# Optimization experiments

Measured on AMD Instinct MI355X. Metric: run time of the kernel, lower is better.

The kernel has to match this reference:

```python
import jax, jax.numpy as jnp
import numpy as np

N_HEAD = 16
T_THRESHOLD = 0.001


def setup_inputs() -> dict:
    key = jax.random.key(0)
    k_x, k_wa, k_ba, k_wp, k_bp = jax.random.split(key, 5)
    B, P, L, R = 8, 1024, 4, 256
    C = L * R  # n_embd = 1024
    s = 1.0 / np.sqrt(C)
    return {
        "x": jax.random.normal(k_x, (B, P, L, R), dtype=jnp.float32),
        "w_attn": jax.random.normal(k_wa, (C, 3 * C), dtype=jnp.float32) * s,
        "b_attn": jax.random.normal(k_ba, (3 * C,), dtype=jnp.float32) * 0.01,
        "w_proj": jax.random.normal(k_wp, (C, C), dtype=jnp.float32) * s,
        "b_proj": jax.random.normal(k_bp, (C,), dtype=jnp.float32) * 0.01,
    }


def reference(x, w_attn, b_attn, w_proj, b_proj):
    B, P, L, R = x.shape
    C = L * R
    H = N_HEAD
    hd = C // H
    xf = x.reshape(B, P, C)                      # (B, T, C)
    qkv = xf @ w_attn + b_attn                   # (B, T, 3C)
    q, k, v = jnp.split(qkv, 3, axis=-1)
    # (B, H, T, hd)
    q = q.reshape(B, P, H, hd).transpose(0, 2, 1, 3)
    k = k.reshape(B, P, H, hd).transpose(0, 2, 1, 3)
    v = v.reshape(B, P, H, hd).transpose(0, 2, 1, 3)
    att = jnp.einsum("bhqd,bhkd->bhqk", q, k) * (1.0 / np.sqrt(hd))
    att = jax.nn.softmax(att, axis=-1)
    att = jax.nn.relu(att - T_THRESHOLD)         # post-softmax thresholding
    y = jnp.einsum("bhqk,bhkd->bhqd", att, v)    # (B, H, T, hd)
    y = y.transpose(0, 2, 1, 3).reshape(B, P, C)
    y = y @ w_proj + b_proj
    return y.reshape(B, P, L, R)
```

## Files before the change

kernel.cpp:

```cpp
#include <hip/hip_runtime.h>


typedef _Float16 half8 __attribute__((ext_vector_type(8)));
typedef _Float16 half4_t __attribute__((ext_vector_type(4)));
typedef float floatx4 __attribute__((ext_vector_type(4)));

__device__ __forceinline__ void gl2lds16(const void* gsrc, void* lds) {
    __builtin_amdgcn_global_load_lds(
        (const __attribute__((address_space(1))) unsigned int*)gsrc,
        (__attribute__((address_space(3))) unsigned int*)lds,
        16, 0, 0);
}

__global__ __launch_bounds__(256) void conv_x(const float4* __restrict__ in,
                                              _Float16* __restrict__ out, int n4) {
    int idx = blockIdx.x * blockDim.x + threadIdx.x;
    int stride = gridDim.x * blockDim.x;
    for (int i = idx; i < n4; i += stride) {
        float4 v = in[i];
        half4_t h = { (_Float16)v.x, (_Float16)v.y, (_Float16)v.z, (_Float16)v.w };
        *(half4_t*)(out + (size_t)i * 4) = h;
    }
}

__global__ __launch_bounds__(256) void tconv2(const float* __restrict__ wa,
                                              _Float16* __restrict__ waT,
                                              const float* __restrict__ wp,
                                              _Float16* __restrict__ wpT) {
    __shared__ _Float16 t[64 * 65];
    int bx = blockIdx.x, by = blockIdx.y;
    const float* in = wa; _Float16* out = waT; int C = 3072;
    if (bx >= 48) { bx -= 48; in = wp; out = wpT; C = 1024; }
#pragma unroll
    for (int it = 0; it < 16; ++it) {
        int idx = it * 256 + threadIdx.x;
        int r = idx >> 6, c = idx & 63;
        t[c * 65 + r] = (_Float16)in[(size_t)(by * 64 + r) * C + bx * 64 + c];
    }
    __syncthreads();
#pragma unroll
    for (int it = 0; it < 16; ++it) {
        int idx = it * 256 + threadIdx.x;
        int rn = idx >> 6, ck = idx & 63;
        out[(size_t)(bx * 64 + rn) * 1024 + by * 64 + ck] = t[rn * 65 + ck];
    }
}

#define GBAR __builtin_amdgcn_s_barrier()
#define WLGKM do { asm volatile("s_waitcnt lgkmcnt(0)" ::: "memory"); } while (0)
#define WVM2  do { asm volatile("s_waitcnt vmcnt(2)"   ::: "memory"); } while (0)
#define WVM4  do { asm volatile("s_waitcnt vmcnt(4)"   ::: "memory"); } while (0)
#define WVM0  do { asm volatile("s_waitcnt vmcnt(0)"   ::: "memory"); } while (0)


#define WLDA(buf, rg)                                                                         \
    do {                                                                                      \
        _Pragma("unroll") for (int i = 0; i < 4; ++i) {                                       \
            int r_ = wm * 128 + ((rg) * 4 + i) * 16 + l15;                                    \
            _Pragma("unroll") for (int kk = 0; kk < 2; ++kk)                                  \
                a[i][kk] = *(const half8*)(sA + (buf) * 32768 + r_ * 128 +                    \
                                           ((((kk << 2) + quad) ^ (r_ & 7)) << 4));           \
        }                                                                                     \
    } while (0)

#define WLDB(buf, cg, bb)                                                                     \
    do {                                                                                      \
        _Pragma("unroll") for (int j = 0; j < 2; ++j) {                                       \
            int r_ = wn * 64 + ((cg) * 2 + j) * 16 + l15;                                     \
            _Pragma("unroll") for (int kk = 0; kk < 2; ++kk)                                  \
                bb[j][kk] = *(const half8*)(sB + (buf) * 32768 + r_ * 128 +                   \
                                            ((((kk << 2) + quad) ^ (r_ & 7)) << 4));          \
        }                                                                                     \
    } while (0)

#define WMMA(rg, cg, bb)                                                                      \
    do {                                                                                      \
        __builtin_amdgcn_s_setprio(1);                                                        \
        _Pragma("unroll") for (int kk = 0; kk < 2; ++kk)                                      \
            _Pragma("unroll") for (int i = 0; i < 4; ++i)                                     \
                _Pragma("unroll") for (int j = 0; j < 2; ++j)                                  \
                    acc[(rg) * 4 + i][(cg) * 2 + j] = __builtin_amdgcn_mfma_f32_16x16x32_f16( \
                        a[i][kk], bb[j][kk], acc[(rg) * 4 + i][(cg) * 2 + j], 0, 0, 0);       \
        __builtin_amdgcn_s_setprio(0);                                                        \
    } while (0)

__global__ __launch_bounds__(512, 2) void gemm_qkv(const _Float16* __restrict__ A,
                                                   const _Float16* __restrict__ BT,
                                                   const float* __restrict__ bias,
                                                   _Float16* __restrict__ qno,
                                                   _Float16* __restrict__ kPo,
                                                   _Float16* __restrict__ vPo) {
    __shared__ __attribute__((aligned(16))) char lds[131072];
    char* sA = lds;
    char* sB = lds + 65536;
    int tid = threadIdx.x;
    int W = tid >> 6, lane = tid & 63, quad = lane >> 4, l15 = lane & 15;
    int wm = W >> 2, wn = W & 3;
    int m0 = blockIdx.y * 256, n0 = blockIdx.x * 256;

    auto stA = [&](int buf, int half, int k0) {
#pragma unroll
        for (int rnd = 0; rnd < 2; ++rnd) {
            int c = rnd * 512 + tid;
            int row = c >> 3;
            int q = (c & 7) ^ (row & 7);
            const _Float16* src = A + (size_t)(m0 + half * 128 + row) * 1024 + k0 + q * 8;
            int off = __builtin_amdgcn_readfirstlane(buf * 32768 + half * 16384 +
                                                     rnd * 8192 + (W << 10));
            gl2lds16(src, sA + off);
        }
    };
    auto stB = [&](int buf, int half, int k0) {
#pragma unroll
        for (int rnd = 0; rnd < 2; ++rnd) {
            int c = rnd * 512 + tid;
            int row = c >> 3;
            int q = (c & 7) ^ (row & 7);
            const _Float16* src = BT + (size_t)(n0 + half * 128 + row) * 1024 + k0 + q * 8;
            int off = __builtin_amdgcn_readfirstlane(buf * 32768 + half * 16384 +
                                                     rnd * 8192 + (W << 10));
            gl2lds16(src, sB + off);
        }
    };

    half8 a[4][2], b0[2][2], b1[2][2];
    floatx4 acc[8][4] = {};

    stA(0, 0, 0); stA(0, 1, 0);
    stB(0, 0, 0); stB(0, 1, 0);
    stB(1, 0, 64); stB(1, 1, 64);
    WVM4;
    GBAR;

#pragma unroll 1
    for (int t = 0; t < 16; t += 2) {
        int k1 = (t + 1) << 6;
        int k2 = ((t + 2) & 15) << 6;
        int k3 = ((t + 3) & 15) << 6;
        WLDA(0, 0); WLDB(0, 0, b0); stA(1, 0, k1);
        GBAR; WLGKM; WMMA(0, 0, b0); GBAR;
        WLDB(0, 1, b1); stA(1, 1, k1);
        GBAR; WLGKM; WMMA(0, 1, b1); GBAR;
        WLDA(0, 1); stB(0, 0, k2);
        GBAR; WLGKM; WMMA(1, 1, b1); GBAR;
        stB(0, 1, k2); WVM4;
        GBAR; WLGKM; WMMA(1, 0, b0); GBAR;
        WLDA(1, 0); WLDB(1, 0, b0); stA(0, 0, k2);
        GBAR; WLGKM; WMMA(0, 0, b0); GBAR;
        WLDB(1, 1, b1); stA(0, 1, k2);
        GBAR; WLGKM; WMMA(0, 1, b1); GBAR;
        WLDA(1, 1); stB(1, 0, k3);
        GBAR; WLGKM; WMMA(1, 1, b1); GBAR;
        stB(1, 1, k3); WVM4;
        GBAR; WLGKM; WMMA(1, 0, b0); GBAR;
    }

    WVM0;
    GBAR;
    int sec = n0 >> 10;
    int b = m0 >> 10;
    int tb = m0 & 1023;
#pragma unroll 1
    for (int p = 0; p < 2; ++p) {
        if (p) __syncthreads();
        if (sec == 2) {
            if ((wn >> 1) == p) {
#pragma unroll
                for (int cf = 0; cf < 4; ++cf) {
                    int lc = (wn & 1) * 64 + cf * 16 + l15;
                    float bv = bias[n0 + wn * 64 + cf * 16 + l15];
#pragma unroll
                    for (int rf = 0; rf < 8; ++rf) {
                        int m = wm * 128 + rf * 16 + quad * 4;
                        half4_t h4;
#pragma unroll
                        for (int r = 0; r < 4; ++r) h4[r] = (_Float16)(acc[rf][cf][r] + bv);
                        *(half4_t*)(lds + lc * 528 + m * 2) = h4;
                    }
                }
            }
            __syncthreads();
            int l15v = tid & 15;
            int moct = W * 4 + ((tid >> 4) & 3);
            int t = tb + moct * 8;
            int kbv = (t >> 5) & 31, quad_v = (t >> 3) & 3;
            int nbV = (n0 & 1023) + p * 128;
#pragma unroll
            for (int i = 0; i < 8; ++i) {
                int hh = i >> 2, cf = i & 3;
                int n = hh * 64 + cf * 16 + l15v;
                half8 v = *(const half8*)(lds + n * 528 + (moct << 4));
                int gcol = nbV + n;
                int h = gcol >> 6, d = gcol & 63;
                size_t chunk = (size_t)((b * 16 + h) * 32 + kbv) * 256 +
                               (d >> 4) * 64 + quad_v * 16 + (d & 15);
                *(half8*)(vPo + chunk * 8) = v;
            }
        } else {
            if ((wn >> 1) == p) {
#pragma unroll
                for (int cf = 0; cf < 4; ++cf) {
                    int lc = (wn & 1) * 64 + cf * 16 + l15;
                    float bv = bias[n0 + wn * 64 + cf * 16 + l15];
#pragma unroll
                    for (int rf = 0; rf < 8; ++rf) {
                        int m = wm * 128 + rf * 16 + quad * 4;
#pragma unroll
                        for (int r = 0; r < 4; ++r)
                            *(_Float16*)(lds + (m + r) * 272 + lc * 2) =
                                (_Float16)(acc[rf][cf][r] + bv);
                    }
                }
            }
            __syncthreads();
            int nb = (n0 & 1023) + p * 128;
            if (sec == 0) {
                int noct = tid & 15;
#pragma unroll
                for (int i = 0; i < 8; ++i) {
                    int m = i * 32 + (tid >> 4);
                    half8 v = *(const half8*)(lds + m * 272 + (noct << 4));
                    *(half8*)(qno + (size_t)(b * 1024 + tb + m) * 1024 + nb + noct * 8) = v;
                }
            } else {
                int l15k = tid & 15, noct = (tid >> 4) & 15;
#pragma unroll
                for (int i = 0; i < 8; ++i) {
                    int mb = i * 2 + (tid >> 8);
                    int m = mb * 16 + l15k;
                    half8 v = *(const half8*)(lds + m * 272 + (noct << 4));
                    int gcol = nb + noct * 8;
                    int h = gcol >> 6, d0 = gcol & 63;
                    int t = tb + m;
                    size_t chunk = (size_t)((b * 16 + h) * 64 + (t >> 4)) * 128 +
                                   (d0 >> 5) * 64 + ((d0 >> 3) & 3) * 16 + l15k;
                    *(half8*)(kPo + chunk * 8) = v;
                }
            }
        }
    }
}

#define LDA(buf, rg)                                                                          \
    do {                                                                                      \
        _Pragma("unroll") for (int i = 0; i < 2; ++i) {                                       \
            int r_ = wm * 64 + ((rg) * 2 + i) * 16 + l15;                                     \
            _Pragma("unroll") for (int kk = 0; kk < 2; ++kk)                                  \
                a[i][kk] = *(const half8*)(sA + (buf) * 32768 + r_ * 128 +                    \
                                           ((((kk << 2) + quad) ^ (r_ & 7)) << 4));           \
        }                                                                                     \
    } while (0)

#define LDB(buf, cg, bb)                                                                      \
    do {                                                                                      \
        _Pragma("unroll") for (int j = 0; j < 2; ++j) {                                       \
            int r_ = wn * 64 + ((cg) * 2 + j) * 16 + l15;                                     \
            _Pragma("unroll") for (int kk = 0; kk < 2; ++kk)                                  \
                bb[j][kk] = *(const half8*)(sB + (buf) * 16384 + r_ * 128 +                   \
                                            ((((kk << 2) + quad) ^ (r_ & 7)) << 4));          \
        }                                                                                     \
    } while (0)

#define MMA(rg, cg, bb)                                                                       \
    do {                                                                                      \
        __builtin_amdgcn_s_setprio(1);                                                        \
        _Pragma("unroll") for (int kk = 0; kk < 2; ++kk)                                      \
            _Pragma("unroll") for (int i = 0; i < 2; ++i)                                     \
                _Pragma("unroll") for (int j = 0; j < 2; ++j)                                  \
                    acc[(rg) * 2 + i][(cg) * 2 + j] = __builtin_amdgcn_mfma_f32_16x16x32_f16( \
                        a[i][kk], bb[j][kk], acc[(rg) * 2 + i][(cg) * 2 + j], 0, 0, 0);       \
        __builtin_amdgcn_s_setprio(0);                                                        \
    } while (0)

__global__ __launch_bounds__(512, 2) void gemm_proj(const _Float16* __restrict__ A,
                                                    const _Float16* __restrict__ BT,
                                                    const float* __restrict__ bias,
                                                    float* __restrict__ o0, int N) {
    __shared__ __attribute__((aligned(16))) char lds[98304];
    char* sA = lds;
    char* sB = lds + 65536;
    int tid = threadIdx.x;
    int W = tid >> 6, lane = tid & 63, quad = lane >> 4, l15 = lane & 15;
    int wm = W >> 1, wn = W & 1;
    int m0 = blockIdx.y * 256, n0 = blockIdx.x * 128;

    auto stA = [&](int buf, int half, int k0) {
#pragma unroll
        for (int rnd = 0; rnd < 2; ++rnd) {
            int c = rnd * 512 + tid;
            int row = c >> 3;
            int q = (c & 7) ^ (row & 7);
            const _Float16* src = A + (size_t)(m0 + half * 128 + row) * 1024 + k0 + q * 8;
            int off = __builtin_amdgcn_readfirstlane(buf * 32768 + half * 16384 +
                                                     rnd * 8192 + (W << 10));
            gl2lds16(src, sA + off);
        }
    };
    auto stB = [&](int buf, int half, int k0) {
        int row = tid >> 3;
        int q = (tid & 7) ^ (row & 7);
        const _Float16* src = BT + (size_t)(n0 + half * 64 + row) * 1024 + k0 + q * 8;
        int off = __builtin_amdgcn_readfirstlane(buf * 16384 + half * 8192 + (W << 10));
        gl2lds16(src, sB + off);
    };

    half8 a[2][2], b0[2][2], b1[2][2];
    floatx4 acc[4][4] = {};

    stA(0, 0, 0); stA(0, 1, 0);
    stB(0, 0, 0); stB(0, 1, 0);
    stB(1, 0, 64); stB(1, 1, 64);
    WVM2;
    GBAR;

#pragma unroll 1
    for (int t = 0; t < 16; t += 2) {
        int k1 = (t + 1) << 6;
        int k2 = ((t + 2) & 15) << 6;
        int k3 = ((t + 3) & 15) << 6;
        LDA(0, 0); LDB(0, 0, b0); stA(1, 0, k1);
        GBAR; WLGKM; MMA(0, 0, b0); GBAR;
        LDB(0, 1, b1); stA(1, 1, k1);
        GBAR; WLGKM; MMA(0, 1, b1); GBAR;
        LDA(0, 1); stB(0, 0, k2);
        GBAR; WLGKM; MMA(1, 1, b1); GBAR;
        stB(0, 1, k2); WVM2;
        GBAR; WLGKM; MMA(1, 0, b0); GBAR;
        LDA(1, 0); LDB(1, 0, b0); stA(0, 0, k2);
        GBAR; WLGKM; MMA(0, 0, b0); GBAR;
        LDB(1, 1, b1); stA(0, 1, k2);
        GBAR; WLGKM; MMA(0, 1, b1); GBAR;
        LDA(1, 1); stB(1, 0, k3);
        GBAR; WLGKM; MMA(1, 1, b1); GBAR;
        stB(1, 1, k3); WVM2;
        GBAR; WLGKM; MMA(1, 0, b0); GBAR;
    }

#pragma unroll
    for (int cf = 0; cf < 4; ++cf) {
        int gn = n0 + wn * 64 + cf * 16 + l15;
        float bv = bias[gn];
#pragma unroll
        for (int rf = 0; rf < 4; ++rf) {
            int gmBase = m0 + wm * 64 + rf * 16 + quad * 4;
#pragma unroll
            for (int r = 0; r < 4; ++r)
                o0[(size_t)(gmBase + r) * N + gn] = acc[rf][cf][r] + bv;
        }
    }
}

__device__ __forceinline__ int esw(int row, int colByte) {
    return row * 2048 + (colByte ^ ((row & 7) << 4));
}

__global__ __launch_bounds__(512, 4) void attn(const _Float16* __restrict__ qn,
                                               const _Float16* __restrict__ kP,
                                               const _Float16* __restrict__ vP,
                                               _Float16* __restrict__ y) {
    __shared__ __attribute__((aligned(16))) _Float16 E[32 * 1024];
    __shared__ float lsum[8][32];
    char* Eb = (char*)E;
    int tid = threadIdx.x;
    int W = tid >> 6, lane = tid & 63, quad = lane >> 4, l15 = lane & 15;
    int flat = blockIdx.y * 32 + blockIdx.x;
    int swz = (flat & 7) * 512 + (flat >> 3);
    int qt = swz & 31, bh = swz >> 5;
    int b = bh >> 4, h = bh & 15;
    int q0 = qt * 32;

    half8 bq[2][2];
#pragma unroll
    for (int nf = 0; nf < 2; ++nf)
#pragma unroll
        for (int ks = 0; ks < 2; ++ks)
            bq[nf][ks] = *(const half8*)(qn + (size_t)(b * 1024 + q0 + nf * 16 + l15) * 1024 +
                                         h * 64 + ks * 32 + quad * 8);

    float lpart[2] = {0.f, 0.f};
#pragma unroll 4
    for (int mt = 0; mt < 8; ++mt) {
        int kb = W * 8 + mt;
        const _Float16* kp = kP + ((size_t)(bh * 64 + kb) * 128 + lane) * 8;
        half8 ak0 = *(const half8*)(kp);
        half8 ak1 = *(const half8*)(kp + 512);
#pragma unroll
        for (int nf = 0; nf < 2; ++nf) {
            floatx4 s = {};
            s = __builtin_amdgcn_mfma_f32_16x16x32_f16(ak0, bq[nf][0], s, 0, 0, 0);
            s = __builtin_amdgcn_mfma_f32_16x16x32_f16(ak1, bq[nf][1], s, 0, 0, 0);
            half4_t h4;
#pragma unroll
            for (int r = 0; r < 4; ++r) {
                float e = __builtin_amdgcn_exp2f(fminf(s[r] * 0.18033688f, 14.4269504f));
                lpart[nf] += e;
                h4[r] = (_Float16)e;
            }
            int q = nf * 16 + l15;
            int kbyte = (W * 128 + mt * 16 + quad * 4) * 2;
            *(half4_t*)(Eb + q * 2048 + (kbyte ^ ((q & 7) << 4))) = h4;
        }
    }
#pragma unroll
    for (int nf = 0; nf < 2; ++nf) {
        lpart[nf] += __shfl_xor(lpart[nf], 16);
        lpart[nf] += __shfl_xor(lpart[nf], 32);
    }
    if (lane < 16) {
        lsum[W][l15] = lpart[0];
        lsum[W][16 + l15] = lpart[1];
    }
    __syncthreads();

    half8 inv8[2], t8, z8;
#pragma unroll
    for (int j = 0; j < 8; ++j) { t8[j] = (_Float16)(-0.001f); z8[j] = (_Float16)0.f; }
#pragma unroll
    for (int rf = 0; rf < 2; ++rf) {
        float l = 0.f;
#pragma unroll
        for (int w = 0; w < 8; ++w) l += lsum[w][rf * 16 + l15];
        _Float16 invh = (_Float16)(1.0f / l);
#pragma unroll
        for (int j = 0; j < 8; ++j) inv8[rf][j] = invh;
    }

    floatx4 acc[2][4] = {};
#pragma unroll
    for (int kt = 0; kt < 4; ++kt) {
        int kk = W * 128 + kt * 32;
        half8 ap[2];
#pragma unroll
        for (int rf = 0; rf < 2; ++rf) {
            ap[rf] = *(const half8*)(Eb + esw(rf * 16 + l15, (kk + quad * 8) * 2));
            ap[rf] = ap[rf] * inv8[rf] + t8;
            ap[rf] = __builtin_elementwise_max(ap[rf], z8);
        }
        const _Float16* vbase = vP + ((size_t)(bh * 32 + (W * 4 + kt)) * 256 + lane) * 8;
        half8 bv[4];
#pragma unroll
        for (int cf = 0; cf < 4; ++cf)
            bv[cf] = *(const half8*)(vbase + cf * 512);
#pragma unroll
        for (int rf = 0; rf < 2; ++rf)
#pragma unroll
            for (int cf = 0; cf < 4; ++cf)
                acc[rf][cf] = __builtin_amdgcn_mfma_f32_16x16x32_f16(ap[rf], bv[cf], acc[rf][cf], 0, 0, 0);
    }
    __syncthreads();

    float* red = (float*)E;
#pragma unroll
    for (int rf = 0; rf < 2; ++rf)
#pragma unroll
        for (int cf = 0; cf < 4; ++cf)
#pragma unroll
            for (int r = 0; r < 4; ++r)
                red[W * 2048 + (rf * 16 + quad * 4 + r) * 64 + cf * 16 + l15] = acc[rf][cf][r];
    __syncthreads();
    {
        int e4 = tid * 4;
        int r = e4 >> 6, c = e4 & 63;
        floatx4 s = {};
#pragma unroll
        for (int w = 0; w < 8; ++w) s += *(const floatx4*)(red + w * 2048 + e4);
        half4_t hv = { (_Float16)s[0], (_Float16)s[1], (_Float16)s[2], (_Float16)s[3] };
        *(half4_t*)(y + (size_t)(b * 1024 + q0 + r) * 1024 + h * 64 + c) = hv;
    }
}

extern "C" void kernel_launch(void* const* d_in, const int* in_sizes, int n_in,
                              void* d_out, int out_size, void* d_ws, size_t ws_size,
                              hipStream_t stream) {
    const float* x  = (const float*)d_in[0];
    const float* wa = (const float*)d_in[1];
    const float* ba = (const float*)d_in[2];
    const float* wp = (const float*)d_in[3];
    const float* bp = (const float*)d_in[4];
    float* out = (float*)d_out;

    char* ws = (char*)d_ws;
    _Float16* y   = (_Float16*)(ws);
    _Float16* qn  = (_Float16*)(ws + 16777216);
    _Float16* kP  = (_Float16*)(ws + 33554432);
    _Float16* vP  = (_Float16*)(ws + 50331648);
    _Float16* waT = (_Float16*)(ws + 67108864);
    _Float16* wpT = (_Float16*)(ws + 73400320);
    _Float16* xh  = (_Float16*)(ws + 75497472);

    conv_x<<<4096, 256, 0, stream>>>((const float4*)x, xh, 8388608 / 4);
    tconv2<<<dim3(64, 16), 256, 0, stream>>>(wa, waT, wp, wpT);
    gemm_qkv<<<dim3(12, 32), 512, 0, stream>>>(xh, waT, ba, qn, kP, vP);
    attn<<<dim3(32, 128), 512, 0, stream>>>(qn, kP, vP, y);
    gemm_proj<<<dim3(8, 32), 512, 0, stream>>>(y, wpT, bp, out, 1024);
}
```

Measured before the change: 258.3 us.

## Fuse prep kernels, swizzle GEMM tiles, prefetch K/V and drop a barrier in attention

The x conversion and the weight transposes are merged into one prep launch, which saves a kernel launch. Both GEMMs remap block IDs with an XCD-style swizzle so that neighbouring tiles land on the same chiplet and share L2. The attention kernel loads all K fragments before the QK^T loop and all V fragments right after the softmax barrier, which hides global latency. It also splits the exp-sum into two chains and removes one __syncthreads before the cross-wave reduction by writing partials into a layout that does not conflict. This raises register pressure, and removing the barrier relies on the E buffer reads having finished.

New measurement: 244.3 us. -5.4%, faster.

```diff
diff --git a/kernel.cpp b/kernel.cpp
--- a/kernel.cpp
+++ b/kernel.cpp
@@ -12,37 +12,40 @@
         16, 0, 0);
 }
 
-__global__ __launch_bounds__(256) void conv_x(const float4* __restrict__ in,
-                                              _Float16* __restrict__ out, int n4) {
-    int idx = blockIdx.x * blockDim.x + threadIdx.x;
-    int stride = gridDim.x * blockDim.x;
-    for (int i = idx; i < n4; i += stride) {
-        float4 v = in[i];
-        half4_t h = { (_Float16)v.x, (_Float16)v.y, (_Float16)v.z, (_Float16)v.w };
-        *(half4_t*)(out + (size_t)i * 4) = h;
-    }
-}
-
-__global__ __launch_bounds__(256) void tconv2(const float* __restrict__ wa,
-                                              _Float16* __restrict__ waT,
-                                              const float* __restrict__ wp,
-                                              _Float16* __restrict__ wpT) {
+__global__ __launch_bounds__(256) void prep(const float4* __restrict__ x4,
+                                            _Float16* __restrict__ xh,
+                                            const float* __restrict__ wa,
+                                            _Float16* __restrict__ waT,
+                                            const float* __restrict__ wp,
+                                            _Float16* __restrict__ wpT) {
     __shared__ _Float16 t[64 * 65];
-    int bx = blockIdx.x, by = blockIdx.y;
-    const float* in = wa; _Float16* out = waT; int C = 3072;
-    if (bx >= 48) { bx -= 48; in = wp; out = wpT; C = 1024; }
-#pragma unroll
-    for (int it = 0; it < 16; ++it) {
-        int idx = it * 256 + threadIdx.x;
-        int r = idx >> 6, c = idx & 63;
-        t[c * 65 + r] = (_Float16)in[(size_t)(by * 64 + r) * C + bx * 64 + c];
-    }
-    __syncthreads();
-#pragma unroll
-    for (int it = 0; it < 16; ++it) {
-        int idx = it * 256 + threadIdx.x;
-        int rn = idx >> 6, ck = idx & 63;
-        out[(size_t)(bx * 64 + rn) * 1024 + by * 64 + ck] = t[rn * 65 + ck];
+    int bid = blockIdx.x;
+    if (bid < 4096) {
+        int idx = bid * 256 + threadIdx.x;
+#pragma unroll
+        for (int i = idx; i < 2097152; i += 1048576) {
+            float4 v = x4[i];
+            half4_t h = { (_Float16)v.x, (_Float16)v.y, (_Float16)v.z, (_Float16)v.w };
+            *(half4_t*)(xh + (size_t)i * 4) = h;
+        }
+    } else {
+        int tt = bid - 4096;
+        int by = tt & 15, bx = tt >> 4;
+        const float* in = wa; _Float16* out = waT; int C = 3072;
+        if (bx >= 48) { bx -= 48; in = wp; out = wpT; C = 1024; }
+#pragma unroll
+        for (int it = 0; it < 16; ++it) {
+            int idx = it * 256 + threadIdx.x;
+            int r = idx >> 6, c = idx & 63;
+            t[c * 65 + r] = (_Float16)in[(size_t)(by * 64 + r) * C + bx * 64 + c];
+        }
+        __syncthreads();
+#pragma unroll
+        for (int it = 0; it < 16; ++it) {
+            int idx = it * 256 + threadIdx.x;
+            int rn = idx >> 6, ck = idx & 63;
+            out[(size_t)(bx * 64 + rn) * 1024 + by * 64 + ck] = t[rn * 65 + ck];
+        }
     }
 }
 
@@ -96,7 +99,9 @@
     int tid = threadIdx.x;
     int W = tid >> 6, lane = tid & 63, quad = lane >> 4, l15 = lane & 15;
     int wm = W >> 2, wn = W & 3;
-    int m0 = blockIdx.y * 256, n0 = blockIdx.x * 256;
+    int flat = blockIdx.y * 12 + blockIdx.x;
+    int swz = (flat & 7) * 48 + (flat >> 3);
+    int m0 = (swz / 12) * 256, n0 = (swz % 12) * 256;
 
     auto stA = [&](int buf, int half, int k0) {
 #pragma unroll
@@ -282,7 +287,9 @@
     int tid = threadIdx.x;
     int W = tid >> 6, lane = tid & 63, quad = lane >> 4, l15 = lane & 15;
     int wm = W >> 1, wn = W & 1;
-    int m0 = blockIdx.y * 256, n0 = blockIdx.x * 128;
+    int flat = blockIdx.y * 8 + blockIdx.x;
+    int swz = (flat & 7) * 32 + (flat >> 3);
+    int m0 = (swz >> 3) * 256, n0 = (swz & 7) * 128;
 
     auto stA = [&](int buf, int half, int k0) {
 #pragma unroll
@@ -377,25 +384,31 @@
             bq[nf][ks] = *(const half8*)(qn + (size_t)(b * 1024 + q0 + nf * 16 + l15) * 1024 +
                                          h * 64 + ks * 32 + quad * 8);
 
-    float lpart[2] = {0.f, 0.f};
-#pragma unroll 4
+    half8 ak[8][2];
+#pragma unroll
     for (int mt = 0; mt < 8; ++mt) {
-        int kb = W * 8 + mt;
-        const _Float16* kp = kP + ((size_t)(bh * 64 + kb) * 128 + lane) * 8;
-        half8 ak0 = *(const half8*)(kp);
-        half8 ak1 = *(const half8*)(kp + 512);
+        const _Float16* kp = kP + ((size_t)(bh * 64 + W * 8 + mt) * 128 + lane) * 8;
+        ak[mt][0] = *(const half8*)(kp);
+        ak[mt][1] = *(const half8*)(kp + 512);
+    }
+    float lp0[2] = {0.f, 0.f}, lp1[2] = {0.f, 0.f};
+#pragma unroll
+    for (int mt = 0; mt < 8; ++mt) {
 #pragma unroll
         for (int nf = 0; nf < 2; ++nf) {
             floatx4 s = {};
-            s = __builtin_amdgcn_mfma_f32_16x16x32_f16(ak0, bq[nf][0], s, 0, 0, 0);
-            s = __builtin_amdgcn_mfma_f32_16x16x32_f16(ak1, bq[nf][1], s, 0, 0, 0);
+            s = __builtin_amdgcn_mfma_f32_16x16x32_f16(ak[mt][0], bq[nf][0], s, 0, 0, 0);
+            s = __builtin_amdgcn_mfma_f32_16x16x32_f16(ak[mt][1], bq[nf][1], s, 0, 0, 0);
             half4_t h4;
+            float esum0 = 0.f, esum1 = 0.f;
 #pragma unroll
             for (int r = 0; r < 4; ++r) {
                 float e = __builtin_amdgcn_exp2f(fminf(s[r] * 0.18033688f, 14.4269504f));
-                lpart[nf] += e;
+                if (r & 1) esum1 += e; else esum0 += e;
                 h4[r] = (_Float16)e;
             }
+            lp0[nf] += esum0;
+            lp1[nf] += esum1;
             int q = nf * 16 + l15;
             int kbyte = (W * 128 + mt * 16 + quad * 4) * 2;
             *(half4_t*)(Eb + q * 2048 + (kbyte ^ ((q & 7) << 4))) = h4;
@@ -403,15 +416,21 @@
     }
 #pragma unroll
     for (int nf = 0; nf < 2; ++nf) {
-        lpart[nf] += __shfl_xor(lpart[nf], 16);
-        lpart[nf] += __shfl_xor(lpart[nf], 32);
-    }
-    if (lane < 16) {
-        lsum[W][l15] = lpart[0];
-        lsum[W][16 + l15] = lpart[1];
+        float lp = lp0[nf] + lp1[nf];
+        lp += __shfl_xor(lp, 16);
+        lp += __shfl_xor(lp, 32);
+        if (lane < 16) lsum[W][nf * 16 + l15] = lp;
     }
     __syncthreads();
 
+    half8 bv[4][4];
+#pragma unroll
+    for (int kt = 0; kt < 4; ++kt) {
+        const _Float16* vbase = vP + ((size_t)(bh * 32 + (W * 4 + kt)) * 256 + lane) * 8;
+#pragma unroll
+        for (int cf = 0; cf < 4; ++cf)
+            bv[kt][cf] = *(const half8*)(vbase + cf * 512);
+    }
     half8 inv8[2], t8, z8;
 #pragma unroll
     for (int j = 0; j < 8; ++j) { t8[j] = (_Float16)(-0.001f); z8[j] = (_Float16)0.f; }
@@ -436,34 +455,30 @@
             ap[rf] = ap[rf] * inv8[rf] + t8;
             ap[rf] = __builtin_elementwise_max(ap[rf], z8);
         }
-        const _Float16* vbase = vP + ((size_t)(bh * 32 + (W * 4 + kt)) * 256 + lane) * 8;
-        half8 bv[4];
+#pragma unroll
+        for (int rf = 0; rf < 2; ++rf)
+#pragma unroll
+            for (int cf = 0; cf < 4; ++cf)
+                acc[rf][cf] = __builtin_amdgcn_mfma_f32_16x16x32_f16(ap[rf], bv[kt][cf], acc[rf][cf], 0, 0, 0);
+    }
+
+#pragma unroll
+    for (int rf = 0; rf < 2; ++rf)
 #pragma unroll
         for (int cf = 0; cf < 4; ++cf)
-            bv[cf] = *(const half8*)(vbase + cf * 512);
-#pragma unroll
-        for (int rf = 0; rf < 2; ++rf)
-#pragma unroll
-            for (int cf = 0; cf < 4; ++cf)
-                acc[rf][cf] = __builtin_amdgcn_mfma_f32_16x16x32_f16(ap[rf], bv[cf], acc[rf][cf], 0, 0, 0);
-    }
-    __syncthreads();
-
-    float* red = (float*)E;
-#pragma unroll
-    for (int rf = 0; rf < 2; ++rf)
-#pragma unroll
-        for (int cf = 0; cf < 4; ++cf)
-#pragma unroll
-            for (int r = 0; r < 4; ++r)
-                red[W * 2048 + (rf * 16 + quad * 4 + r) * 64 + cf * 16 + l15] = acc[rf][cf][r];
+#pragma unroll
+            for (int r = 0; r < 4; ++r) {
+                int row = rf * 16 + quad * 4 + r;
+                *(float*)(Eb + row * 2048 + W * 256 + (cf * 16 + l15) * 4) = acc[rf][cf][r];
+            }
     __syncthreads();
     {
         int e4 = tid * 4;
         int r = e4 >> 6, c = e4 & 63;
         floatx4 s = {};
 #pragma unroll
-        for (int w = 0; w < 8; ++w) s += *(const floatx4*)(red + w * 2048 + e4);
+        for (int w = 0; w < 8; ++w)
+            s += *(const floatx4*)(Eb + r * 2048 + w * 256 + c * 4);
         half4_t hv = { (_Float16)s[0], (_Float16)s[1], (_Float16)s[2], (_Float16)s[3] };
         *(half4_t*)(y + (size_t)(b * 1024 + q0 + r) * 1024 + h * 64 + c) = hv;
     }
@@ -488,8 +503,7 @@
     _Float16* wpT = (_Float16*)(ws + 73400320);
     _Float16* xh  = (_Float16*)(ws + 75497472);
 
-    conv_x<<<4096, 256, 0, stream>>>((const float4*)x, xh, 8388608 / 4);
-    tconv2<<<dim3(64, 16), 256, 0, stream>>>(wa, waT, wp, wpT);
+    prep<<<5120, 256, 0, stream>>>((const float4*)x, xh, wa, waT, wp, wpT);
     gemm_qkv<<<dim3(12, 32), 512, 0, stream>>>(xh, waT, ba, qn, kP, vP);
     attn<<<dim3(32, 128), 512, 0, stream>>>(qn, kP, vP, y);
     gemm_proj<<<dim3(8, 32), 512, 0, stream>>>(y, wpT, bp, out, 1024);
```
